# Performance work log

Measured on AMD Instinct MI355X. Metric: run time of the kernel, lower is better.

Reference implementation:

```python
import jax, jax.numpy as jnp
import numpy as np

MODEL_DIM = 2048
Q_HEADS = 32
KV_HEADS = 8
HEAD_DIM = MODEL_DIM // Q_HEADS  # 64
ROPE_BASE = 10000.0


def apply_rope(x, pos):
    # x: [B, S, H, D], interleaved-pair RoPE (torchtune-style)
    half = x.shape[-1] // 2
    inv_freq = 1.0 / (ROPE_BASE ** (jnp.arange(half, dtype=jnp.float32) * 2.0 / x.shape[-1]))
    ang = pos.astype(jnp.float32)[:, None] * inv_freq[None, :]        # [S, half]
    cos = jnp.cos(ang)[None, :, None, :]                              # [1,S,1,half]
    sin = jnp.sin(ang)[None, :, None, :]
    x1 = x[..., 0::2]
    x2 = x[..., 1::2]
    o1 = x1 * cos - x2 * sin
    o2 = x2 * cos + x1 * sin
    return jnp.stack([o1, o2], axis=-1).reshape(x.shape)


def setup_inputs() -> dict:
    key = jax.random.key(0)
    ks = jax.random.split(key, 5)
    B, S, D = 2, 2048, MODEL_DIM
    sd = 1.0 / np.sqrt(D)
    x = jax.random.normal(ks[0], (B, S, D), dtype=jnp.float32)
    wq = jax.random.normal(ks[1], (Q_HEADS * HEAD_DIM, D), dtype=jnp.float32) * sd
    wk = jax.random.normal(ks[2], (KV_HEADS * HEAD_DIM, D), dtype=jnp.float32) * sd
    wv = jax.random.normal(ks[3], (KV_HEADS * HEAD_DIM, D), dtype=jnp.float32) * sd
    wo = jax.random.normal(ks[4], (D, D), dtype=jnp.float32) * sd
    attention_mask = jnp.ones((B, S), dtype=bool)
    return {"x": x, "attention_mask": attention_mask, "wq": wq, "wk": wk, "wv": wv, "wo": wo}


def reference(x, attention_mask, wq, wk, wv, wo):
    B, S, D = x.shape
    rep = Q_HEADS // KV_HEADS
    q = (x @ wq.T).reshape(B, S, Q_HEADS, HEAD_DIM)
    k = (x @ wk.T).reshape(B, S, KV_HEADS, HEAD_DIM)
    v = (x @ wv.T).reshape(B, S, KV_HEADS, HEAD_DIM)
    # GQA repeat_interleave along head axis
    k = jnp.repeat(k, rep, axis=2)
    v = jnp.repeat(v, rep, axis=2)
    pos = jnp.arange(S)
    q = apply_rope(q, pos)
    k = apply_rope(k, pos)
    # scores [B, H, Sq, Sk]
    score = jnp.einsum('bqhd,bkhd->bhqk', q, k) / np.sqrt(HEAD_DIM)
    neg_inf = jnp.finfo(score.dtype).min
    causal = jnp.tril(jnp.ones((S, S), dtype=bool))
    score = jnp.where(causal[None, None, :, :], score, neg_inf)
    score = jnp.where(attention_mask[:, None, None, :], score, neg_inf)
    attn = jax.nn.softmax(score, axis=-1)
    out = jnp.einsum('bhqk,bkhd->bqhd', attn, v).reshape(B, S, D)
    return out @ wo.T
```

## Files before the change

### kernel.cpp

```cpp
#include <hip/hip_runtime.h>
#include <hip/hip_bf16.h>

#define S_LEN 2048
#define BATCH 2
#define DMODEL 2048
#define HQ 32
#define HKV 8
#define HD 64
#define NQ 2560
#define KDIM 2048

typedef __attribute__((ext_vector_type(8))) short bf16x8;
typedef __attribute__((ext_vector_type(4))) float f32x4;

#if __has_builtin(__builtin_amdgcn_exp2f)
#define EXP2(x) __builtin_amdgcn_exp2f(x)
#else
#define EXP2(x) exp2f(x)
#endif

static __device__ inline ushort f2bf(float f) {
    union { float f; unsigned u; } v; v.f = f;
    unsigned r = v.u + 0x7fff + ((v.u >> 16) & 1);
    return (ushort)(r >> 16);
}
static __device__ inline float bf2f(ushort h) {
    union { unsigned u; float f; } v; v.u = ((unsigned)h) << 16; return v.f;
}
static __device__ inline unsigned pack2(float lo, float hi) {
    return (unsigned)f2bf(lo) | ((unsigned)f2bf(hi) << 16);
}
static __device__ __forceinline__ unsigned pkbf(float lo, float hi) {
    union { float f; unsigned u; } a, b; a.f = lo; b.f = hi;
    return __builtin_amdgcn_perm(b.u + 0x8000u, a.u + 0x8000u, 0x07060302u);
}

static __device__ __forceinline__ void gload16(const ushort* g, ushort* l) {
    __builtin_amdgcn_global_load_lds(
        (const __attribute__((address_space(1))) unsigned int*)(g),
        (__attribute__((address_space(3))) unsigned int*)(l), 16, 0, 0);
}

__global__ __launch_bounds__(256) void convert_kernel(const float* __restrict__ x,
                                                      const float* __restrict__ wq,
                                                      const float* __restrict__ wk,
                                                      const float* __restrict__ wv,
                                                      const float* __restrict__ wo,
                                                      ushort* __restrict__ xb,
                                                      ushort* __restrict__ wqkvb,
                                                      ushort* __restrict__ wob)
{
    size_t e = ((size_t)blockIdx.x * 256 + threadIdx.x) * 8;
    const float* src; ushort* dst;
    if (e < 8388608ul)       { src = x  + e;              dst = xb + e; }
    else if (e < 12582912ul) { src = wq + (e - 8388608);  dst = wqkvb + (e - 8388608); }
    else if (e < 13631488ul) { src = wk + (e - 12582912); dst = wqkvb + 4194304 + (e - 12582912); }
    else if (e < 14680064ul) { src = wv + (e - 13631488); dst = wqkvb + 5242880 + (e - 13631488); }
    else                     { src = wo + (e - 14680064); dst = wob + (e - 14680064); }
    float4 a = *(const float4*)src;
    float4 b = *(const float4*)(src + 4);
    uint4 p; p.x = pack2(a.x, a.y); p.y = pack2(a.z, a.w);
             p.z = pack2(b.x, b.y); p.w = pack2(b.z, b.w);
    *(uint4*)dst = p;
}

__global__ __launch_bounds__(256) void gemm_qkv(const ushort* __restrict__ A,
                                                const ushort* __restrict__ Bw,
                                                ushort* __restrict__ qkv,
                                                ushort* __restrict__ vT)
{
    __shared__ ushort As[128 * 32];
    __shared__ ushort Bs[128 * 32];
    const int t    = threadIdx.x;
    const int w    = t >> 6, lane = t & 63;
    const int quad = lane >> 4, l15 = lane & 15;
    const int nb   = blockIdx.x * 128, mb = blockIdx.y * 128;
    const int wm   = (w >> 1) * 64, wn = (w & 1) * 64;
    const int srow = (lane >> 2);
    const int scol = (lane & 3) * 8;

    f32x4 acc[4][4] = {};
    for (int kb = 0; kb < KDIM; kb += 32) {
        __syncthreads();
        #pragma unroll
        for (int c = 0; c < 2; c++) {
            int row = w * 32 + c * 16 + srow;
            gload16(A  + (size_t)(mb + row) * KDIM + kb + scol, &As[(w * 32 + c * 16) * 32]);
            gload16(Bw + (size_t)(nb + row) * KDIM + kb + scol, &Bs[(w * 32 + c * 16) * 32]);
        }
        __syncthreads();
        bf16x8 af[4], bf[4];
        #pragma unroll
        for (int i = 0; i < 4; i++) af[i] = *(const bf16x8*)&As[(wm + i * 16 + l15) * 32 + quad * 8];
        #pragma unroll
        for (int j = 0; j < 4; j++) bf[j] = *(const bf16x8*)&Bs[(wn + j * 16 + l15) * 32 + quad * 8];
        #pragma unroll
        for (int i = 0; i < 4; i++)
            #pragma unroll
            for (int j = 0; j < 4; j++)
                acc[i][j] = __builtin_amdgcn_mfma_f32_16x16x32_bf16(af[i], bf[j], acc[i][j], 0, 0, 0);
    }
    #pragma unroll
    for (int i = 0; i < 4; i++)
        #pragma unroll
        for (int j = 0; j < 4; j++) {
            int n0 = nb + wn + j * 16;
            int m0 = mb + wm + i * 16 + quad * 4;
            if (n0 >= 2560) {
                ushort4 pk;
                pk.x = f2bf(acc[i][j][0]); pk.y = f2bf(acc[i][j][1]);
                pk.z = f2bf(acc[i][j][2]); pk.w = f2bf(acc[i][j][3]);
                *(ushort4*)&vT[(size_t)(n0 + l15 - 2560) * 4096 + m0] = pk;
            } else {
                #pragma unroll
                for (int r = 0; r < 4; r++)
                    qkv[(size_t)(m0 + r) * NQ + n0 + l15] = f2bf(acc[i][j][r]);
            }
        }
}

__global__ __launch_bounds__(256) void rope_kernel(ushort* __restrict__ qkv)
{
    const int PAIRS = BATCH * S_LEN * (HQ + HKV) * (HD / 2);
    int tid = blockIdx.x * 256 + threadIdx.x;
    if (tid >= PAIRS) return;
    int token = tid / ((HQ + HKV) * 32);
    int r     = tid - token * ((HQ + HKV) * 32);
    int hh    = r >> 5;
    int i     = r & 31;
    int base  = (hh < HQ) ? hh * 64 : DMODEL + (hh - HQ) * 64;
    size_t addr = (size_t)token * NQ + base + 2 * i;
    int s = token & (S_LEN - 1);
    float freq = exp2f(-0.41524101186092f * (float)i);
    float ang  = (float)s * freq;
    float sn, cs;
    sincosf(ang, &sn, &cs);
    float x1 = bf2f(qkv[addr]);
    float x2 = bf2f(qkv[addr + 1]);
    qkv[addr]     = f2bf(x1 * cs - x2 * sn);
    qkv[addr + 1] = f2bf(x2 * cs + x1 * sn);
}

__global__ __launch_bounds__(256) void attn_kernel(const ushort* __restrict__ qkv,
                                                   const ushort* __restrict__ vT,
                                                   ushort* __restrict__ attnb)
{
    __shared__ ushort Ks[2][64 * 64];
    __shared__ ushort VT[2][64 * 64];
    __shared__ ushort PT[4][32 * 72];
    const int t    = threadIdx.x;
    const int w    = t >> 6, lane = t & 63;
    const int quad = lane >> 4, l15 = lane & 15;
    const int bid  = blockIdx.x;
    const int qx   = 15 - (bid >> 6);
    const int h    = bid & 31;
    const int b    = (bid >> 5) & 1;
    const int qb   = qx * 128;
    const int kvh  = h >> 2;
    const ushort* base = qkv + (size_t)b * S_LEN * NQ;
    const ushort* vTb  = vT + (size_t)kvh * HD * 4096 + b * S_LEN;

    const float SC = 0.18033688011112042f;
    bf16x8 aq[2][2];
    #pragma unroll
    for (int h2 = 0; h2 < 2; h2++) {
        const ushort* qp = base + (size_t)(qb + w * 32 + h2 * 16 + l15) * NQ + h * HD + quad * 8;
        #pragma unroll
        for (int hf = 0; hf < 2; hf++) {
            bf16x8 v = *(const bf16x8*)(qp + hf * 32);
            #pragma unroll
            for (int j = 0; j < 8; j++) v[j] = (short)f2bf(bf2f((ushort)v[j]) * SC);
            aq[h2][hf] = v;
        }
    }

    f32x4 o[2][4] = {};
    float lsum[2] = {};
    const int qw    = qb + w * 32;
    const int strow = lane >> 3;
    const int stlc  = (lane & 7) ^ strow;
    ushort* ptw = &PT[w][0];
    const int niter = (qb + 128) / 64;

    #pragma unroll
    for (int c = 0; c < 2; c++) {
        int key = w * 16 + c * 8 + strow;
        gload16(base + (size_t)key * NQ + DMODEL + kvh * HD + stlc * 8,
                &Ks[0][(w * 16 + c * 8) * 64]);
        gload16(vTb + (size_t)key * 4096 + stlc * 8,
                &VT[0][(w * 16 + c * 8) * 64]);
    }

    for (int i = 0; i < niter; i++) {
        const int kb  = i * 64;
        const int cur = i & 1;
        __syncthreads();
        if (i + 1 < niter) {
            int kb2 = kb + 64;
            #pragma unroll
            for (int c = 0; c < 2; c++) {
                int key = w * 16 + c * 8 + strow;
                gload16(base + (size_t)(kb2 + key) * NQ + DMODEL + kvh * HD + stlc * 8,
                        &Ks[1 - cur][(w * 16 + c * 8) * 64]);
                gload16(vTb + (size_t)key * 4096 + kb2 + stlc * 8,
                        &VT[1 - cur][(w * 16 + c * 8) * 64]);
            }
        }
        if (kb <= qw + 31) {
            const bool full = (kb + 63) <= qw;
            const ushort* ks = &Ks[cur][0];
            const ushort* vs = &VT[cur][0];
            f32x4 s[2][4];
            #pragma unroll
            for (int kt = 0; kt < 4; kt++) {
                int key = kt * 16 + l15;
                int sw  = l15 & 7;
                bf16x8 k0 = *(const bf16x8*)&ks[key * 64 + (quad ^ sw) * 8];
                bf16x8 k1 = *(const bf16x8*)&ks[key * 64 + (((quad + 4) & 7) ^ sw) * 8];
                #pragma unroll
                for (int h2 = 0; h2 < 2; h2++) {
                    f32x4 z = {};
                    z = __builtin_amdgcn_mfma_f32_16x16x32_bf16(k0, aq[h2][0], z, 0, 0, 0);
                    z = __builtin_amdgcn_mfma_f32_16x16x32_bf16(k1, aq[h2][1], z, 0, 0, 0);
                    s[h2][kt] = z;
                }
            }
            #pragma unroll
            for (int h2 = 0; h2 < 2; h2++) {
                int rq    = h2 * 16 + l15;
                int wbase = rq * 72 + (quad & 1) * 4;
                #pragma unroll
                for (int kt = 0; kt < 4; kt++) {
                    float p0 = EXP2(s[h2][kt][0]);
                    float p1 = EXP2(s[h2][kt][1]);
                    float p2 = EXP2(s[h2][kt][2]);
                    float p3 = EXP2(s[h2][kt][3]);
                    if (!full) {
                        int key0 = kb + kt * 16 + quad * 4;
                        int q    = qb + w * 32 + rq;
                        p0 = (key0 + 0 <= q) ? p0 : 0.f;
                        p1 = (key0 + 1 <= q) ? p1 : 0.f;
                        p2 = (key0 + 2 <= q) ? p2 : 0.f;
                        p3 = (key0 + 3 <= q) ? p3 : 0.f;
                    }
                    lsum[h2] += (p0 + p1) + (p2 + p3);
                    int pc = kt * 2 + (quad >> 1);
                    uint2 pk;
                    pk.x = pkbf(p0, p1);
                    pk.y = pkbf(p2, p3);
                    *(uint2*)&ptw[wbase + pc * 8] = pk;
                }
            }
            bf16x8 pf[2][2];
            #pragma unroll
            for (int h2 = 0; h2 < 2; h2++) {
                int rq = h2 * 16 + l15;
                #pragma unroll
                for (int kc = 0; kc < 2; kc++)
                    pf[h2][kc] = *(const bf16x8*)&ptw[rq * 72 + (kc * 4 + quad) * 8];
            }
            #pragma unroll
            for (int tt = 0; tt < 4; tt++) {
                int dr = tt * 16 + l15;
                int sw = l15 & 7;
                bf16x8 vf0 = *(const bf16x8*)&vs[dr * 64 + (quad ^ sw) * 8];
                bf16x8 vf1 = *(const bf16x8*)&vs[dr * 64 + (((quad + 4) & 7) ^ sw) * 8];
                #pragma unroll
                for (int h2 = 0; h2 < 2; h2++) {
                    f32x4 oo = o[h2][tt];
                    oo = __builtin_amdgcn_mfma_f32_16x16x32_bf16(vf0, pf[h2][0], oo, 0, 0, 0);
                    oo = __builtin_amdgcn_mfma_f32_16x16x32_bf16(vf1, pf[h2][1], oo, 0, 0, 0);
                    o[h2][tt] = oo;
                }
            }
        }
    }
    #pragma unroll
    for (int h2 = 0; h2 < 2; h2++) {
        float l = lsum[h2];
        l += __shfl_xor(l, 16, 64);
        l += __shfl_xor(l, 32, 64);
        float inv = 1.0f / l;
        ushort* ob = attnb + (size_t)(b * S_LEN + qb + w * 32 + h2 * 16 + l15) * DMODEL
                   + h * HD + quad * 4;
        #pragma unroll
        for (int tt = 0; tt < 4; tt++) {
            uint2 st;
            st.x = pkbf(o[h2][tt][0] * inv, o[h2][tt][1] * inv);
            st.y = pkbf(o[h2][tt][2] * inv, o[h2][tt][3] * inv);
            *(uint2*)&ob[tt * 16] = st;
        }
    }
}

__global__ __launch_bounds__(256) void gemm_out(const ushort* __restrict__ A,
                                                const ushort* __restrict__ Bw,
                                                float* __restrict__ C)
{
    __shared__ ushort As[128 * 32];
    __shared__ ushort Bs[128 * 32];
    const int t    = threadIdx.x;
    const int w    = t >> 6, lane = t & 63;
    const int quad = lane >> 4, l15 = lane & 15;
    const int nb   = blockIdx.x * 128, mb = blockIdx.y * 128;
    const int wm   = (w >> 1) * 64, wn = (w & 1) * 64;
    const int srow = (lane >> 2);
    const int scol = (lane & 3) * 8;

    f32x4 acc[4][4] = {};
    for (int kb = 0; kb < KDIM; kb += 32) {
        __syncthreads();
        #pragma unroll
        for (int c = 0; c < 2; c++) {
            int row = w * 32 + c * 16 + srow;
            gload16(A  + (size_t)(mb + row) * KDIM + kb + scol, &As[(w * 32 + c * 16) * 32]);
            gload16(Bw + (size_t)(nb + row) * KDIM + kb + scol, &Bs[(w * 32 + c * 16) * 32]);
        }
        __syncthreads();
        bf16x8 af[4], bf[4];
        #pragma unroll
        for (int i = 0; i < 4; i++) af[i] = *(const bf16x8*)&As[(wm + i * 16 + l15) * 32 + quad * 8];
        #pragma unroll
        for (int j = 0; j < 4; j++) bf[j] = *(const bf16x8*)&Bs[(wn + j * 16 + l15) * 32 + quad * 8];
        #pragma unroll
        for (int i = 0; i < 4; i++)
            #pragma unroll
            for (int j = 0; j < 4; j++)
                acc[i][j] = __builtin_amdgcn_mfma_f32_16x16x32_bf16(af[i], bf[j], acc[i][j], 0, 0, 0);
    }
    #pragma unroll
    for (int i = 0; i < 4; i++)
        #pragma unroll
        for (int j = 0; j < 4; j++)
            #pragma unroll
            for (int r = 0; r < 4; r++) {
                int m = mb + wm + i * 16 + quad * 4 + r;
                int n = nb + wn + j * 16 + l15;
                C[(size_t)m * DMODEL + n] = acc[i][j][r];
            }
}

extern "C" void kernel_launch(void* const* d_in, const int* in_sizes, int n_in,
                              void* d_out, int out_size, void* d_ws, size_t ws_size,
                              hipStream_t stream)
{
    const float* x  = (const float*)d_in[0];
    const float* wq = (const float*)d_in[2];
    const float* wk = (const float*)d_in[3];
    const float* wv = (const float*)d_in[4];
    const float* wo = (const float*)d_in[5];
    float* out = (float*)d_out;

    char* ws = (char*)d_ws;
    ushort* qkv    = (ushort*)(ws);
    ushort* vT     = (ushort*)(ws + 20971520);
    ushort* xb     = (ushort*)(ws + 25165824);
    ushort* attn_b = xb;
    ushort* wqkvb  = (ushort*)(ws + 41943040);
    ushort* wob    = (ushort*)(ws + 54525952);

    convert_kernel<<<9216, 256, 0, stream>>>(x, wq, wk, wv, wo, xb, wqkvb, wob);

    gemm_qkv<<<dim3(3072 / 128, 4096 / 128), 256, 0, stream>>>(xb, wqkvb, qkv, vT);

    int pairs = BATCH * S_LEN * (HQ + HKV) * (HD / 2);
    rope_kernel<<<(pairs + 255) / 256, 256, 0, stream>>>(qkv);

    attn_kernel<<<1024, 256, 0, stream>>>(qkv, vT, attn_b);

    gemm_out<<<dim3(DMODEL / 128, 4096 / 128), 256, 0, stream>>>(attn_b, wob, out);
}
```

Measured before the change: 300.4 us.

## Replace GEMMs with 256x256 double-buffered swizzled-LDS pipelined MFMA kernel

Both projection GEMMs move from a 128x128 tile with K-step 32 and full syncs to a shared templated 256x256 tile kernel with 8 waves, K-step 64, double-buffered LDS, XOR-swizzled LDS layout, explicit vmcnt waits and barriers interleaving loads with MFMA, s_setprio, and a workgroup remap for L2 locality. The goal is more data reuse per tile, hidden global-load latency, and fewer LDS bank conflicts. In exchange each block uses 128KB of LDS and there are only 192 and 128 workgroups, which may underfill the GPU's CUs.

```diff
diff --git a/kernel.cpp b/kernel.cpp
--- a/kernel.cpp
+++ b/kernel.cpp
@@ -40,6 +40,9 @@
         (const __attribute__((address_space(1))) unsigned int*)(g),
         (__attribute__((address_space(3))) unsigned int*)(l), 16, 0, 0);
 }
+
+#define BARRIER() asm volatile("s_barrier" ::: "memory")
+#define WAITVM(N) asm volatile("s_waitcnt vmcnt(" #N ")" ::: "memory")
 
 __global__ __launch_bounds__(256) void convert_kernel(const float* __restrict__ x,
                                                       const float* __restrict__ wq,
@@ -64,59 +67,151 @@
     *(uint4*)dst = p;
 }
 
-__global__ __launch_bounds__(256) void gemm_qkv(const ushort* __restrict__ A,
-                                                const ushort* __restrict__ Bw,
-                                                ushort* __restrict__ qkv,
-                                                ushort* __restrict__ vT)
+template<int NTX, int EPI>
+__global__ __launch_bounds__(512, 2) void gemm256(const ushort* __restrict__ A,
+                                                  const ushort* __restrict__ Bw,
+                                                  ushort* __restrict__ qkv,
+                                                  ushort* __restrict__ vT,
+                                                  float* __restrict__ Cf)
 {
-    __shared__ ushort As[128 * 32];
-    __shared__ ushort Bs[128 * 32];
+    __shared__ ushort As[2][256 * 64];
+    __shared__ ushort Bs[2][256 * 64];
     const int t    = threadIdx.x;
     const int w    = t >> 6, lane = t & 63;
     const int quad = lane >> 4, l15 = lane & 15;
-    const int nb   = blockIdx.x * 128, mb = blockIdx.y * 128;
-    const int wm   = (w >> 1) * 64, wn = (w & 1) * 64;
-    const int srow = (lane >> 2);
-    const int scol = (lane & 3) * 8;
-
-    f32x4 acc[4][4] = {};
-    for (int kb = 0; kb < KDIM; kb += 32) {
-        __syncthreads();
-        #pragma unroll
-        for (int c = 0; c < 2; c++) {
-            int row = w * 32 + c * 16 + srow;
-            gload16(A  + (size_t)(mb + row) * KDIM + kb + scol, &As[(w * 32 + c * 16) * 32]);
-            gload16(Bw + (size_t)(nb + row) * KDIM + kb + scol, &Bs[(w * 32 + c * 16) * 32]);
-        }
-        __syncthreads();
-        bf16x8 af[4], bf[4];
-        #pragma unroll
-        for (int i = 0; i < 4; i++) af[i] = *(const bf16x8*)&As[(wm + i * 16 + l15) * 32 + quad * 8];
-        #pragma unroll
-        for (int j = 0; j < 4; j++) bf[j] = *(const bf16x8*)&Bs[(wn + j * 16 + l15) * 32 + quad * 8];
+    const int l8   = lane >> 3;
+    const int scw  = ((lane & 7) ^ (l8 & 7)) * 8;
+    const int wm   = (w >> 2) * 128;
+    const int wn   = (w & 3) * 64;
+
+    const int nwg = NTX * 16;
+    int bid = blockIdx.x;
+    int sb  = (bid & 7) * (nwg >> 3) + (bid >> 3);
+    const int mb = (sb / NTX) * 256;
+    const int nb = (sb % NTX) * 256;
+
+    f32x4 acc[8][4] = {};
+    bf16x8 a[4][2], b0[2][2], b1[2][2];
+
+    auto SA = [&](int buf, int half, int kb) {
+        #pragma unroll
+        for (int L = 0; L < 2; L++) {
+            int r0 = half * 128 + (w * 2 + L) * 8;
+            gload16(A + (size_t)(mb + r0 + l8) * KDIM + kb + scw, &As[buf][r0 * 64]);
+        }
+    };
+    auto SB = [&](int buf, int half, int kb) {
+        #pragma unroll
+        for (int L = 0; L < 2; L++) {
+            int r0 = half * 128 + (w * 2 + L) * 8;
+            gload16(Bw + (size_t)(nb + r0 + l8) * KDIM + kb + scw, &Bs[buf][r0 * 64]);
+        }
+    };
+    auto LA = [&](int buf, int hm) {
+        #pragma unroll
+        for (int i = 0; i < 4; i++) {
+            int r = wm + hm * 64 + i * 16 + l15;
+            int rs = r * 64, sw = r & 7;
+            #pragma unroll
+            for (int kc = 0; kc < 2; kc++)
+                a[i][kc] = *(const bf16x8*)&As[buf][rs + (((kc << 2) | quad) ^ sw) * 8];
+        }
+    };
+    auto LB = [&](int buf, int hn, bf16x8 (&b)[2][2]) {
+        #pragma unroll
+        for (int j = 0; j < 2; j++) {
+            int r = wn + hn * 32 + j * 16 + l15;
+            int rs = r * 64, sw = r & 7;
+            #pragma unroll
+            for (int kc = 0; kc < 2; kc++)
+                b[j][kc] = *(const bf16x8*)&Bs[buf][rs + (((kc << 2) | quad) ^ sw) * 8];
+        }
+    };
+    auto MM = [&](bf16x8 (&b)[2][2], int hm, int hn) {
+        __builtin_amdgcn_s_setprio(1);
         #pragma unroll
         for (int i = 0; i < 4; i++)
             #pragma unroll
-            for (int j = 0; j < 4; j++)
-                acc[i][j] = __builtin_amdgcn_mfma_f32_16x16x32_bf16(af[i], bf[j], acc[i][j], 0, 0, 0);
-    }
+            for (int j = 0; j < 2; j++) {
+                f32x4 d = acc[hm * 4 + i][hn * 2 + j];
+                d = __builtin_amdgcn_mfma_f32_16x16x32_bf16(a[i][0], b[j][0], d, 0, 0, 0);
+                d = __builtin_amdgcn_mfma_f32_16x16x32_bf16(a[i][1], b[j][1], d, 0, 0, 0);
+                acc[hm * 4 + i][hn * 2 + j] = d;
+            }
+        __builtin_amdgcn_s_setprio(0);
+    };
+
+    SA(0, 0, 0);  SA(0, 1, 0);  SB(0, 0, 0);  SB(0, 1, 0);
+    SA(1, 0, 64); SA(1, 1, 64); SB(1, 0, 64); SB(1, 1, 64);
+    WAITVM(8);
+    BARRIER();
+
+    #pragma unroll 1
+    for (int it = 0; it < 16; it++) {
+        const int kb2 = it * 128 + 128;
+        const bool pre = (it < 15);
+        LA(0, 0); LB(0, 0, b0);
+        BARRIER();
+        MM(b0, 0, 0);
+        BARRIER();
+        LB(0, 1, b1);
+        BARRIER();
+        MM(b1, 0, 1);
+        BARRIER();
+        LA(0, 1);
+        if (pre) { SB(0, 0, kb2); SB(0, 1, kb2); }
+        BARRIER();
+        MM(b1, 1, 1);
+        BARRIER();
+        if (pre) { SA(0, 0, kb2); SA(0, 1, kb2); }
+        BARRIER();
+        MM(b0, 1, 0);
+        if (pre) { WAITVM(8); } else { WAITVM(0); }
+        BARRIER();
+        LA(1, 0); LB(1, 0, b0);
+        BARRIER();
+        MM(b0, 0, 0);
+        BARRIER();
+        LB(1, 1, b1);
+        BARRIER();
+        MM(b1, 0, 1);
+        BARRIER();
+        LA(1, 1);
+        if (pre) { SB(1, 0, kb2 + 64); SB(1, 1, kb2 + 64); }
+        BARRIER();
+        MM(b1, 1, 1);
+        BARRIER();
+        if (pre) { SA(1, 0, kb2 + 64); SA(1, 1, kb2 + 64); }
+        BARRIER();
+        MM(b0, 1, 0);
+        if (pre) { WAITVM(8); } else { WAITVM(0); }
+        BARRIER();
+    }
+
     #pragma unroll
-    for (int i = 0; i < 4; i++)
+    for (int i = 0; i < 8; i++) {
+        int m0 = mb + wm + (i >> 2) * 64 + (i & 3) * 16 + quad * 4;
         #pragma unroll
         for (int j = 0; j < 4; j++) {
-            int n0 = nb + wn + j * 16;
-            int m0 = mb + wm + i * 16 + quad * 4;
-            if (n0 >= 2560) {
-                ushort4 pk;
-                pk.x = f2bf(acc[i][j][0]); pk.y = f2bf(acc[i][j][1]);
-                pk.z = f2bf(acc[i][j][2]); pk.w = f2bf(acc[i][j][3]);
-                *(ushort4*)&vT[(size_t)(n0 + l15 - 2560) * 4096 + m0] = pk;
+            int n0 = nb + wn + (j >> 1) * 32 + (j & 1) * 16;
+            if (EPI == 0) {
+                if (n0 >= 2560) {
+                    ushort4 pk;
+                    pk.x = f2bf(acc[i][j][0]); pk.y = f2bf(acc[i][j][1]);
+                    pk.z = f2bf(acc[i][j][2]); pk.w = f2bf(acc[i][j][3]);
+                    *(ushort4*)&vT[(size_t)(n0 + l15 - 2560) * 4096 + m0] = pk;
+                } else {
+                    #pragma unroll
+                    for (int r = 0; r < 4; r++)
+                        qkv[(size_t)(m0 + r) * NQ + n0 + l15] = f2bf(acc[i][j][r]);
+                }
             } else {
                 #pragma unroll
                 for (int r = 0; r < 4; r++)
-                    qkv[(size_t)(m0 + r) * NQ + n0 + l15] = f2bf(acc[i][j][r]);
-            }
-        }
+                    Cf[(size_t)(m0 + r) * DMODEL + n0 + l15] = acc[i][j][r];
+            }
+        }
+    }
 }
 
 __global__ __launch_bounds__(256) void rope_kernel(ushort* __restrict__ qkv)
@@ -293,53 +388,6 @@
     }
 }
 
-__global__ __launch_bounds__(256) void gemm_out(const ushort* __restrict__ A,
-                                                const ushort* __restrict__ Bw,
-                                                float* __restrict__ C)
-{
-    __shared__ ushort As[128 * 32];
-    __shared__ ushort Bs[128 * 32];
-    const int t    = threadIdx.x;
-    const int w    = t >> 6, lane = t & 63;
-    const int quad = lane >> 4, l15 = lane & 15;
-    const int nb   = blockIdx.x * 128, mb = blockIdx.y * 128;
-    const int wm   = (w >> 1) * 64, wn = (w & 1) * 64;
-    const int srow = (lane >> 2);
-    const int scol = (lane & 3) * 8;
-
-    f32x4 acc[4][4] = {};
-    for (int kb = 0; kb < KDIM; kb += 32) {
-        __syncthreads();
-        #pragma unroll
-        for (int c = 0; c < 2; c++) {
-            int row = w * 32 + c * 16 + srow;
-            gload16(A  + (size_t)(mb + row) * KDIM + kb + scol, &As[(w * 32 + c * 16) * 32]);
-            gload16(Bw + (size_t)(nb + row) * KDIM + kb + scol, &Bs[(w * 32 + c * 16) * 32]);
-        }
-        __syncthreads();
-        bf16x8 af[4], bf[4];
-        #pragma unroll
-        for (int i = 0; i < 4; i++) af[i] = *(const bf16x8*)&As[(wm + i * 16 + l15) * 32 + quad * 8];
-        #pragma unroll
-        for (int j = 0; j < 4; j++) bf[j] = *(const bf16x8*)&Bs[(wn + j * 16 + l15) * 32 + quad * 8];
-        #pragma unroll
-        for (int i = 0; i < 4; i++)
-            #pragma unroll
-            for (int j = 0; j < 4; j++)
-                acc[i][j] = __builtin_amdgcn_mfma_f32_16x16x32_bf16(af[i], bf[j], acc[i][j], 0, 0, 0);
-    }
-    #pragma unroll
-    for (int i = 0; i < 4; i++)
-        #pragma unroll
-        for (int j = 0; j < 4; j++)
-            #pragma unroll
-            for (int r = 0; r < 4; r++) {
-                int m = mb + wm + i * 16 + quad * 4 + r;
-                int n = nb + wn + j * 16 + l15;
-                C[(size_t)m * DMODEL + n] = acc[i][j][r];
-            }
-}
-
 extern "C" void kernel_launch(void* const* d_in, const int* in_sizes, int n_in,
                               void* d_out, int out_size, void* d_ws, size_t ws_size,
                               hipStream_t stream)
@@ -361,12 +409,12 @@
 
     convert_kernel<<<9216, 256, 0, stream>>>(x, wq, wk, wv, wo, xb, wqkvb, wob);
 
-    gemm_qkv<<<dim3(3072 / 128, 4096 / 128), 256, 0, stream>>>(xb, wqkvb, qkv, vT);
+    gemm256<12, 0><<<192, 512, 0, stream>>>(xb, wqkvb, qkv, vT, nullptr);
 
     int pairs = BATCH * S_LEN * (HQ + HKV) * (HD / 2);
     rope_kernel<<<(pairs + 255) / 256, 256, 0, stream>>>(qkv);
 
     attn_kernel<<<1024, 256, 0, stream>>>(qkv, vT, attn_b);
 
-    gemm_out<<<dim3(DMODEL / 128, 4096 / 128), 256, 0, stream>>>(attn_b, wob, out);
-}
+    gemm256<8, 1><<<128, 512, 0, stream>>>(attn_b, wob, nullptr, nullptr, out);
+}
```

Result: slower. 307.1 us (+2.2%).
